# Performance work log

Measured on AMD Instinct MI355X. Metric: run time of the kernel, lower is better.

Reference implementation:

```python
import jax, jax.numpy as jnp
import numpy as np

B, T, V, K = 4, 1024, 32000, 50000
EPS_T, EPS_M = 1e-8, 1e-12


def setup_inputs() -> dict:
    key = jax.random.key(0)
    k1, k2, k3, k4 = jax.random.split(key, 4)
    probs = jax.random.uniform(k1, (B, T, V), dtype=jnp.float32)
    # normalize so rows are valid distributions (faithful to softmax outputs)
    probs = probs / probs.sum(-1, keepdims=True)
    target_probs = jax.random.uniform(k2, (K,), dtype=jnp.float32) * (1.0 / K)
    target_oov = jax.random.uniform(k3, (1,), dtype=jnp.float32)
    mask = jnp.ones((B, T), dtype=bool)
    pairs = jax.random.randint(k4, (K, 2), 0, V, dtype=jnp.int64 if jax.config.jax_enable_x64 else jnp.int32)
    return {"probs": probs, "target_probs": target_probs, "target_oov": target_oov,
            "mask": mask, "pairs": pairs}


def reference(probs, target_probs, target_oov, mask, pairs):
    a = pairs[:, 0]  # (K,)
    b = pairs[:, 1]
    p_t = probs[:, :-1, :]   # (B, T-1, V)
    p_t1 = probs[:, 1:, :]
    pair_mask = (mask[:, :-1] & mask[:, 1:]).astype(jnp.float32)  # (B, T-1)
    # gather bigram probs: (B, T-1, K) joint, masked sum over batch/seq
    joint = p_t[..., a] * p_t1[..., b]
    topk_sum = jnp.einsum('btk,bt->k', joint, pair_mask)  # (K,)
    n_pairs = pair_mask.sum()

    # finalize
    n = jnp.maximum(n_pairs, 1.0)
    model_top = jnp.maximum(topk_sum / n, EPS_M)
    model_oov = jnp.clip(1.0 - model_top.sum(), EPS_M, 1.0 - EPS_T)
    tgt = jnp.maximum(target_probs, EPS_T)
    t_oov = jnp.maximum(target_oov[0], EPS_T)
    kl_top = (model_top * (jnp.log(model_top) - jnp.log(tgt))).sum()
    kl_oov = model_oov * (jnp.log(model_oov) - jnp.log(t_oov))
    return kl_top + kl_oov
```

## Files before the change

kernel.cpp:

```cpp
#include <hip/hip_runtime.h>
#include <stdint.h>

#define B_   4
#define T_   1024
#define V_   32000
#define K_   50000
#define N_   (B_*(T_-1))
#define TPB  1024
#define U_   49
#define KP   (TPB*U_)
#define POS_PER_BLK 16
#define G1   ((N_ + POS_PER_BLK - 1)/POS_PER_BLK)
#define EPSTGT 1e-8f
#define EPSMOD 1e-12f
#define W4   (V_/4)

__device__ __forceinline__ uint32_t bf16rne(float x) {
    uint32_t u = __float_as_uint(x);
    u += 0x7FFFu + ((u >> 16) & 1u);
    return u >> 16;
}
__device__ __forceinline__ uint2 pack4(float4 v) {
    uint2 pk;
    pk.x = bf16rne(v.x) | (bf16rne(v.y) << 16);
    pk.y = bf16rne(v.z) | (bf16rne(v.w) << 16);
    return pk;
}
__device__ __forceinline__ void stage_row(const float* __restrict__ probs, int r,
                                          ushort* dst, int tid) {
    const float4* src = (const float4*)(probs + (size_t)r * V_);
    for (int i = tid; i < W4; i += TPB) {
        *(uint2*)(dst + i * 4) = pack4(src[i]);
    }
}

#define GATHER(pkv, accv) do {                                          \
    uint32_t ao_ = (pkv) >> 16, bo_ = (pkv) & 0xFFFFu;                  \
    ushort av_ = *(const ushort*)(rp + ao_);                            \
    ushort bv_ = *(const ushort*)(rq + bo_);                            \
    accv = fmaf(__uint_as_float((uint32_t)av_ << 16),                   \
                __uint_as_float((uint32_t)bv_ << 16), accv);            \
} while (0)

__global__ void k_pack(const int* __restrict__ pairs, uint32_t* __restrict__ ppk) {
    int k = blockIdx.x * 256 + threadIdx.x;
    if (k >= KP) return;
    uint32_t v = 0;
    if (k < K_) {
        uint32_t a = (uint32_t)pairs[2 * k];
        uint32_t b = (uint32_t)pairs[2 * k + 1];
        v = ((a * 2u) << 16) | (b * 2u);
    }
    ppk[k] = v;
}

__global__ void k_mask(const unsigned char* __restrict__ mask, float* __restrict__ scalars) {
    __shared__ int red[16];
    int tid = threadIdx.x;
    int cnt = 0;
    for (int n = tid; n < N_; n += 1024) {
        int b = n / (T_ - 1);
        int t = n - b * (T_ - 1);
        int r = b * T_ + t;
        cnt += (mask[r] && mask[r + 1]) ? 1 : 0;
    }
    for (int off = 32; off > 0; off >>= 1) cnt += __shfl_down(cnt, off, 64);
    int wid = tid >> 6, lid = tid & 63;
    if (lid == 0) red[wid] = cnt;
    __syncthreads();
    if (tid == 0) {
        int s = 0;
        for (int w = 0; w < 16; ++w) s += red[w];
        scalars[0] = (float)s;
    }
}

__global__ __launch_bounds__(TPB) void k_main(
    const float* __restrict__ probs,
    const unsigned char* __restrict__ mask,
    const uint32_t* __restrict__ ppk,
    float* __restrict__ partials, int S, int direct)
{
    __shared__ __align__(16) ushort rows[2][V_];
    __shared__ unsigned char mask_s[32];
    const int tid = threadIdx.x;
    const int g = blockIdx.x;
    const int n0 = g * POS_PER_BLK;
    const int n1 = min(N_, n0 + POS_PER_BLK);

    int r0 = n0 + n0 / (T_ - 1);
    int r1 = r0 + 1;
    const int rbase = r0;
    {
        int rlast = (n1 - 1) + (n1 - 1) / (T_ - 1) + 1;
        int nrows = rlast - rbase + 1;
        if (tid < nrows) mask_s[tid] = mask[rbase + tid];
    }

    float acc[U_];
#pragma unroll
    for (int u = 0; u < U_; ++u) acc[u] = 0.f;

    stage_row(probs, r0, rows[r0 & 1], tid);
    stage_row(probs, r1, rows[r1 & 1], tid);

    const uint32_t* pp = ppk + tid;

    for (int n = n0; n < n1; ++n) {
        const int nn = n + 1;
        const bool more = (nn < n1);
        const int nr0 = nn + nn / (T_ - 1);
        const int nr1 = nr0 + 1;
        const int pre_row = more ? ((nr0 == r1) ? nr1 : nr0) : -1;
        const bool extra = more && (nr0 != r1);
        const int ld_row = (pre_row >= 0) ? pre_row : 0;
        const float4* src = (const float4*)(probs + (size_t)ld_row * V_);

        __syncthreads();

        uint32_t pkA[28];
#pragma unroll
        for (int j = 0; j < 28; ++j) pkA[j] = pp[j * TPB];
        __builtin_amdgcn_sched_barrier(0);
        float4 L0[4];
#pragma unroll
        for (int j = 0; j < 4; ++j) L0[j] = src[tid + j * TPB];
        __builtin_amdgcn_sched_barrier(0);

        const bool active = mask_s[r0 - rbase] && mask_s[r1 - rbase];
        const char* rp = (const char*)rows[r0 & 1];
        const char* rq = (const char*)rows[r1 & 1];

        if (active) {
#pragma unroll
            for (int j = 0; j < 14; ++j) GATHER(pkA[j], acc[j]);
        }
        uint32_t pkB[21];
#pragma unroll
        for (int j = 0; j < 21; ++j) pkB[j] = pp[(28 + j) * TPB];
        __builtin_amdgcn_sched_barrier(0);
        if (active) {
#pragma unroll
            for (int j = 14; j < 28; ++j) GATHER(pkA[j], acc[j]);
        }
        uint2 P0[4];
#pragma unroll
        for (int j = 0; j < 4; ++j) P0[j] = pack4(L0[j]);
        float4 L1[4];
#pragma unroll
        for (int j = 0; j < 4; ++j) {
            int i = tid + (4 + j) * TPB;
            L1[j] = src[(i < W4) ? i : 0];
        }
        __builtin_amdgcn_sched_barrier(0);
        if (active) {
#pragma unroll
            for (int j = 0; j < 21; ++j) GATHER(pkB[j], acc[28 + j]);
        }

        __syncthreads();

        if (pre_row >= 0) {
            ushort* dst = rows[pre_row & 1];
#pragma unroll
            for (int j = 0; j < 4; ++j)
                *(uint2*)(dst + (tid + j * TPB) * 4) = P0[j];
#pragma unroll
            for (int j = 0; j < 4; ++j) {
                int i = tid + (4 + j) * TPB;
                if (i < W4) *(uint2*)(dst + i * 4) = pack4(L1[j]);
            }
            if (extra) stage_row(probs, nr1, rows[nr1 & 1], tid);
        }
        r0 = nr0; r1 = nr1;
    }

    if (direct) {
        float* slot = partials + (size_t)g * KP;
#pragma unroll
        for (int u = 0; u < U_; ++u) slot[u * TPB + tid] = acc[u];
    } else {
        float* slot = partials + (size_t)(g % S) * KP;
#pragma unroll
        for (int u = 0; u < U_; ++u) atomicAdd(slot + u * TPB + tid, acc[u]);
    }
}

__global__ void k_reduce(const float* __restrict__ partials, const float* __restrict__ tgt,
                         float* __restrict__ scalars, int S) {
    int k = blockIdx.x * 256 + threadIdx.x;
    float n = fmaxf(scalars[0], 1.0f);
    float mt = 0.f, term = 0.f;
    if (k < K_) {
        float ts = 0.f;
        for (int s = 0; s < S; ++s) ts += partials[(size_t)s * KP + k];
        mt = fmaxf(ts / n, EPSMOD);
        float tg = fmaxf(tgt[k], EPSTGT);
        term = mt * (__logf(mt) - __logf(tg));
    }
    for (int off = 32; off > 0; off >>= 1) {
        mt += __shfl_down(mt, off, 64);
        term += __shfl_down(term, off, 64);
    }
    __shared__ float rm[4], rt[4];
    int wid = threadIdx.x >> 6, lid = threadIdx.x & 63;
    if (lid == 0) { rm[wid] = mt; rt[wid] = term; }
    __syncthreads();
    if (threadIdx.x == 0) {
        float sm = 0.f, st = 0.f;
        for (int w = 0; w < 4; ++w) { sm += rm[w]; st += rt[w]; }
        atomicAdd(&scalars[1], sm);
        atomicAdd(&scalars[2], st);
    }
}

__global__ void k_final(const float* __restrict__ scalars, const float* __restrict__ toov,
                        float* __restrict__ out) {
    float S1 = scalars[1], S2 = scalars[2];
    float moov = 1.f - S1;
    moov = fminf(fmaxf(moov, EPSMOD), 1.f - EPSTGT);
    float tv = fmaxf(toov[0], EPSTGT);
    out[0] = S2 + moov * (__logf(moov) - __logf(tv));
}

extern "C" void kernel_launch(void* const* d_in, const int* in_sizes, int n_in,
                              void* d_out, int out_size, void* d_ws, size_t ws_size,
                              hipStream_t stream) {
    const float* probs = (const float*)d_in[0];
    const float* tgt   = (const float*)d_in[1];
    const float* toov  = (const float*)d_in[2];
    const unsigned char* mask = (const unsigned char*)d_in[3];
    const int* pairs   = (const int*)d_in[4];
    float* out = (float*)d_out;

    char* ws = (char*)d_ws;
    uint32_t* ppk = (uint32_t*)ws;
    size_t off_sc = (size_t)KP * 4;
    float* scalars = (float*)(ws + off_sc);
    size_t off_pt = off_sc + 256;
    float* partials = (float*)(ws + off_pt);

    long avail = (long)ws_size - (long)off_pt;
    int smax = (int)(avail / ((long)KP * 4));
    int direct = (smax >= G1) ? 1 : 0;
    int S = direct ? G1 : (smax < 1 ? 1 : (smax > 64 ? 64 : smax));

    hipMemsetAsync(ws + off_sc, 0, 256, stream);
    if (!direct) hipMemsetAsync(partials, 0, (size_t)S * KP * 4, stream);
    k_pack<<<(KP + 255) / 256, 256, 0, stream>>>(pairs, ppk);
    k_mask<<<1, 1024, 0, stream>>>(mask, scalars);
    k_main<<<G1, TPB, 0, stream>>>(probs, mask, ppk, partials, S, direct);
    k_reduce<<<(K_ + 255) / 256, 256, 0, stream>>>(partials, tgt, scalars, S);
    k_final<<<1, 1, 0, stream>>>(scalars, toov, out);
}
```

Measured before the change: 762.1 us.

## Permute pair order so LDS gathers within a wavefront avoid bank conflicts

A single-block preprocessing kernel bins the K pairs by the LDS bank (word index mod 32) of both gather addresses. It then places them in the packed index array so that each 64-lane wavefront's gathers from each row fall into distinct banks, spilling overflow pairs into leftover holes. The reduction kernel uses a stored permutation to map accumulator slots back to the original pair index for the target lookup. This aims to reduce LDS bank conflicts in the main gather loop. The cost is an extra serial single-block kernel and more workspace.

```diff
diff --git a/kernel.cpp b/kernel.cpp
--- a/kernel.cpp
+++ b/kernel.cpp
@@ -14,6 +14,9 @@
 #define EPSTGT 1e-8f
 #define EPSMOD 1e-12f
 #define W4   (V_/4)
+#define NGRP (KP/64)
+#define SCAP (2*NGRP)
+#define PINV 0xFFFFFFFFu
 
 __device__ __forceinline__ uint32_t bf16rne(float x) {
     uint32_t u = __float_as_uint(x);
@@ -42,16 +45,66 @@
                 __uint_as_float((uint32_t)bv_ << 16), accv);            \
 } while (0)
 
-__global__ void k_pack(const int* __restrict__ pairs, uint32_t* __restrict__ ppk) {
-    int k = blockIdx.x * 256 + threadIdx.x;
-    if (k >= KP) return;
-    uint32_t v = 0;
-    if (k < K_) {
+__global__ __launch_bounds__(1024) void k_perm(const int* __restrict__ pairs,
+                                               uint32_t* __restrict__ ppk,
+                                               uint32_t* __restrict__ perm,
+                                               uint32_t* __restrict__ ovf,
+                                               uint32_t* __restrict__ holes) {
+    __shared__ uint32_t hist[32][32];
+    __shared__ uint32_t boff[32][32];
+    __shared__ uint32_t cnt[32][32];
+    __shared__ uint32_t binc[32], rot[32];
+    __shared__ uint32_t novf, nhole;
+    const int tid = threadIdx.x;
+
+    ((uint32_t*)hist)[tid] = 0;
+    if (tid == 0) { novf = 0; nhole = 0; }
+    __syncthreads();
+
+    for (int k = tid; k < K_; k += 1024) {
         uint32_t a = (uint32_t)pairs[2 * k];
         uint32_t b = (uint32_t)pairs[2 * k + 1];
-        v = ((a * 2u) << 16) | (b * 2u);
-    }
-    ppk[k] = v;
+        atomicAdd(&hist[(a >> 1) & 31][(b >> 1) & 31], 1u);
+    }
+    __syncthreads();
+
+    if (tid < 32) {
+        uint32_t s = 0;
+        for (int j = 0; j < 32; ++j) { boff[tid][j] = s; s += hist[tid][j]; }
+        binc[tid] = s;
+        rot[tid] = ((uint32_t)tid * s) >> 5;
+    }
+    __syncthreads();
+    ((uint32_t*)cnt)[tid] = 0;
+    for (int s = tid; s < KP; s += 1024) { ppk[s] = 0; perm[s] = PINV; }
+    __syncthreads();
+
+    for (int k = tid; k < K_; k += 1024) {
+        uint32_t a = (uint32_t)pairs[2 * k];
+        uint32_t b = (uint32_t)pairs[2 * k + 1];
+        uint32_t aw = (a >> 1) & 31, bw = (b >> 1) & 31;
+        uint32_t j = boff[aw][bw] + atomicAdd(&cnt[aw][bw], 1u);
+        uint32_t c = binc[aw];
+        uint32_t jp = j + rot[aw]; if (jp >= c) jp -= c;
+        uint32_t pk = ((a * 2u) << 16) | (b * 2u);
+        if (jp < SCAP) {
+            uint32_t s = ((jp >> 1) << 6) + aw + ((jp & 1u) << 5);
+            ppk[s] = pk; perm[s] = (uint32_t)k;
+        } else {
+            uint32_t i = atomicAdd(&novf, 1u);
+            ovf[2 * i] = pk; ovf[2 * i + 1] = (uint32_t)k;
+        }
+    }
+    __syncthreads();
+
+    for (int s = tid; s < KP; s += 1024) {
+        if (perm[s] == PINV) { uint32_t i = atomicAdd(&nhole, 1u); holes[i] = (uint32_t)s; }
+    }
+    __syncthreads();
+    for (uint32_t i = tid; i < novf; i += 1024) {
+        uint32_t s = holes[i];
+        ppk[s] = ovf[2 * i]; perm[s] = ovf[2 * i + 1];
+    }
 }
 
 __global__ void k_mask(const unsigned char* __restrict__ mask, float* __restrict__ scalars) {
@@ -186,17 +239,21 @@
     }
 }
 
-__global__ void k_reduce(const float* __restrict__ partials, const float* __restrict__ tgt,
+__global__ void k_reduce(const float* __restrict__ partials, const uint32_t* __restrict__ perm,
+                         const float* __restrict__ tgt,
                          float* __restrict__ scalars, int S) {
-    int k = blockIdx.x * 256 + threadIdx.x;
+    int si = blockIdx.x * 256 + threadIdx.x;
     float n = fmaxf(scalars[0], 1.0f);
     float mt = 0.f, term = 0.f;
-    if (k < K_) {
-        float ts = 0.f;
-        for (int s = 0; s < S; ++s) ts += partials[(size_t)s * KP + k];
-        mt = fmaxf(ts / n, EPSMOD);
-        float tg = fmaxf(tgt[k], EPSTGT);
-        term = mt * (__logf(mt) - __logf(tg));
+    if (si < KP) {
+        uint32_t k = perm[si];
+        if (k != PINV) {
+            float ts = 0.f;
+            for (int s = 0; s < S; ++s) ts += partials[(size_t)s * KP + si];
+            mt = fmaxf(ts / n, EPSMOD);
+            float tg = fmaxf(tgt[k], EPSTGT);
+            term = mt * (__logf(mt) - __logf(tg));
+        }
     }
     for (int off = 32; off > 0; off >>= 1) {
         mt += __shfl_down(mt, off, 64);
@@ -234,8 +291,11 @@
     float* out = (float*)d_out;
 
     char* ws = (char*)d_ws;
-    uint32_t* ppk = (uint32_t*)ws;
-    size_t off_sc = (size_t)KP * 4;
+    uint32_t* ppk   = (uint32_t*)(ws + 0);
+    uint32_t* perm  = (uint32_t*)(ws + 200704);
+    uint32_t* ovf   = (uint32_t*)(ws + 401408);
+    uint32_t* holes = (uint32_t*)(ws + 801536);
+    size_t off_sc = 1002240;
     float* scalars = (float*)(ws + off_sc);
     size_t off_pt = off_sc + 256;
     float* partials = (float*)(ws + off_pt);
@@ -247,9 +307,9 @@
 
     hipMemsetAsync(ws + off_sc, 0, 256, stream);
     if (!direct) hipMemsetAsync(partials, 0, (size_t)S * KP * 4, stream);
-    k_pack<<<(KP + 255) / 256, 256, 0, stream>>>(pairs, ppk);
+    k_perm<<<1, 1024, 0, stream>>>(pairs, ppk, perm, ovf, holes);
     k_mask<<<1, 1024, 0, stream>>>(mask, scalars);
     k_main<<<G1, TPB, 0, stream>>>(probs, mask, ppk, partials, S, direct);
-    k_reduce<<<(K_ + 255) / 256, 256, 0, stream>>>(partials, tgt, scalars, S);
+    k_reduce<<<(KP + 255) / 256, 256, 0, stream>>>(partials, perm, tgt, scalars, S);
     k_final<<<1, 1, 0, stream>>>(scalars, toov, out);
 }
```

Measured after the change: 877.1 us. +15.1%, slower.
